# Kernel tuning notes

Measured on AMD Instinct MI355X. Metric: run time of the kernel, lower is better.

## Reference

```python
import jax, jax.numpy as jnp
import numpy as np

D_MODEL = 2048
NUM_HEADS = 32
D_HEAD = D_MODEL // NUM_HEADS
L = 2048


def setup_inputs() -> dict:
    key = jax.random.key(0)
    ks = jax.random.split(key, 9)
    s = 0.02  # init scale
    return {
        "X": jax.random.normal(ks[0], (L, D_MODEL), dtype=jnp.float32),
        "Wq_w": jax.random.normal(ks[1], (D_MODEL, D_MODEL), jnp.float32) * s,
        "Wq_b": jax.random.normal(ks[2], (D_MODEL,), jnp.float32) * s,
        "Wk_w": jax.random.normal(ks[3], (D_MODEL, D_MODEL), jnp.float32) * s,
        "Wk_b": jax.random.normal(ks[4], (D_MODEL,), jnp.float32) * s,
        "Wv_w": jax.random.normal(ks[5], (D_MODEL, D_MODEL), jnp.float32) * s,
        "Wv_b": jax.random.normal(ks[6], (D_MODEL,), jnp.float32) * s,
        "Wo_w": jax.random.normal(ks[7], (D_MODEL, D_MODEL), jnp.float32) * s,
        "Wo_b": jax.random.normal(ks[8], (D_MODEL,), jnp.float32) * s,
    }


def reference(X, Wq_w, Wq_b, Wk_w, Wk_b, Wv_w, Wv_b, Wo_w, Wo_b):
    # torch.nn.Linear: y = x @ W.T + b
    seq = X.shape[0]
    Q = (X @ Wq_w.T + Wq_b).reshape(seq, D_HEAD, NUM_HEADS)  # (L, d, h)
    K = (X @ Wk_w.T + Wk_b).reshape(seq, D_HEAD, NUM_HEADS)
    V = (X @ Wv_w.T + Wv_b).reshape(seq, D_HEAD, NUM_HEADS)
    # scores[l, m, h] = sum_d Q[l,d,h] * K[m,d,h]; note scale is sqrt(d_model),
    # faithful to the source (not sqrt(d_head)).
    scores = jnp.einsum('ldh,mdh->lmh', Q, K) / jnp.sqrt(jnp.float32(D_MODEL))
    attn = jax.nn.softmax(scores, axis=1)  # softmax over key axis m
    out = jnp.einsum('lmh,mdh->ldh', attn, V).reshape(seq, D_MODEL)
    return out @ Wo_w.T + Wo_b
```

## Files before the change

### kernel.cpp

```cpp
#include <hip/hip_runtime.h>
#include <hip/hip_bf16.h>
#include <stdint.h>
#include <stddef.h>

#define L_SEQ   2048
#define DM      2048
#define NH      32
#define DH      64
#define QSCALE  0.02209708691207961f
#define QS2     0.0318793579f
#define MAT_N   (L_SEQ * DM)

typedef __bf16  bf16x8 __attribute__((ext_vector_type(8)));
typedef float   f32x4  __attribute__((ext_vector_type(4)));
typedef __hip_bfloat16 bf16;

#if __has_builtin(__builtin_amdgcn_exp2f)
#define EXP2F(x) __builtin_amdgcn_exp2f(x)
#else
#define EXP2F(x) __expf((x) * 0.6931471805599453f)
#endif

__device__ __forceinline__ void gl_lds16(const bf16* g, bf16* l) {
    __builtin_amdgcn_global_load_lds(
        (const __attribute__((address_space(1))) unsigned int*)g,
        (__attribute__((address_space(3))) unsigned int*)l,
        16, 0, 0);
}

__device__ __forceinline__ void conv8s(const float* src, bf16* dst, int i, float sc) {
    float4 a = *(const float4*)(src + i);
    float4 b = *(const float4*)(src + i + 4);
    union { bf16 h[8]; uint4 u; } pk;
    pk.h[0] = __float2bfloat16(a.x * sc); pk.h[1] = __float2bfloat16(a.y * sc);
    pk.h[2] = __float2bfloat16(a.z * sc); pk.h[3] = __float2bfloat16(a.w * sc);
    pk.h[4] = __float2bfloat16(b.x * sc); pk.h[5] = __float2bfloat16(b.y * sc);
    pk.h[6] = __float2bfloat16(b.z * sc); pk.h[7] = __float2bfloat16(b.w * sc);
    *(uint4*)(dst + i) = pk.u;
}

__global__ __launch_bounds__(256)
void convert4_kernel(const float* __restrict__ s0, const float* __restrict__ s1,
                     const float* __restrict__ s2, const float* __restrict__ s3,
                     bf16* __restrict__ d0, bf16* __restrict__ d1,
                     bf16* __restrict__ d2, bf16* __restrict__ d3)
{
    const float* s; bf16* d; float sc = 1.0f;
    switch (blockIdx.y) {
        case 0:  s = s0; d = d0; break;
        case 1:  s = s1; d = d1; sc = QS2; break;
        case 2:  s = s2; d = d2; break;
        default: s = s3; d = d3; break;
    }
    const int i = (blockIdx.x * 256 + threadIdx.x) * 8;
    conv8s(s, d, i, sc);
}

__global__ __launch_bounds__(256)
void convert_wo_perm_kernel(const float* __restrict__ s, bf16* __restrict__ d)
{
    const int t   = blockIdx.x * 256 + threadIdx.x;
    const int row = t >> 8;
    const int k0  = (t & 255) * 8;
    const float* sr = s + (size_t)row * DM;
    union { bf16 h[8]; uint4 u; } pk;
#pragma unroll
    for (int j = 0; j < 8; ++j) {
        const int kp = k0 + j;
        const int k  = ((kp & 63) << 5) | (kp >> 6);
        pk.h[j] = __float2bfloat16(sr[k]);
    }
    *(uint4*)(d + (size_t)row * DM + k0) = pk.u;
}

__global__ __launch_bounds__(512)
void qkv8_gemm_kernel(const bf16* __restrict__ Xb,
                      const bf16* __restrict__ Wq, const float* __restrict__ bq,
                      const bf16* __restrict__ Wk, const float* __restrict__ bk,
                      const bf16* __restrict__ Wv, const float* __restrict__ bv,
                      bf16* __restrict__ Qws, bf16* __restrict__ Kws, bf16* __restrict__ Vws)
{
    __shared__ bf16 lds[2 * 32768];

    const int bid = blockIdx.x;
    const int mt  = bid & 7;
    const int nt  = bid >> 3;
    const int m0  = mt << 8;
    const int ng0 = nt << 8;
    const int z   = ng0 >> 11;
    const int n0  = ng0 & 2047;
    const bf16*  W    = (z == 0) ? Wq : (z == 1) ? Wk : Wv;
    const float* bias = (z == 0) ? bq : (z == 1) ? bk : bv;

    const int tid  = threadIdx.x;
    const int lane = tid & 63;
    const int wave = tid >> 6;
    const int wm   = wave >> 2;
    const int wn   = wave & 3;
    const int grp8 = (lane >> 4) * 8;
    const int grp4 = (lane >> 4) * 4;
    const int l15  = lane & 15;
    const int axor = (l15 & 7) << 3;

    const int scol = ((tid & 7) * 8) ^ (((tid >> 3) & 7) << 3);
    const bf16* gb[8];
    int loff[8];
#pragma unroll
    for (int e = 0; e < 8; ++e) {
        const int hh  = e >> 1;
        const int row = (e & 1) * 64 + (tid >> 3);
        loff[e] = hh * 8192 + (e & 1) * 4096 + tid * 8;
        if (hh < 2) {
            gb[e] = Xb + (size_t)(m0 + hh * 128 + row) * DM + scol;
        } else {
            const int nn   = n0 + (hh - 2) * 128 + row;
            const int brow = ((nn & 63) << 5) | (nn >> 6);
            gb[e] = W + (size_t)brow * DM + scol;
        }
    }

    const bool swap  = (z == 2);
    const int  aside = swap ? 16384 : 0;
    const int  bside = swap ? 0 : 16384;
    const bf16* fa0 = lds + aside + wm * 8192 + l15 * 64;
    const bf16* fb0 = lds + bside + (wn >> 1) * 8192 + ((wn & 1) * 64 + l15) * 64;

    f32x4 acc[8][4];
    const f32x4 zero = {0.f, 0.f, 0.f, 0.f};
#pragma unroll
    for (int i = 0; i < 8; ++i)
#pragma unroll
        for (int j = 0; j < 4; ++j) acc[i][j] = zero;

#pragma unroll
    for (int e = 0; e < 8; ++e) gl_lds16(gb[e],      lds + loff[e]);
#pragma unroll
    for (int e = 0; e < 8; ++e) gl_lds16(gb[e] + 64, lds + 32768 + loff[e]);
    asm volatile("s_waitcnt vmcnt(8)" ::: "memory");
    asm volatile("s_barrier" ::: "memory");

    for (int t = 0; t < 32; ++t) {
        const int cb = (t & 1) << 15;
        const bf16* fa = fa0 + cb;
        const bf16* fb = fb0 + cb;
        const int c0 = grp8 ^ axor;
        const int c1 = (32 + grp8) ^ axor;

        bf16x8 af[8], bfr[4];
#pragma unroll
        for (int i = 0; i < 8; ++i) af[i] = *(const bf16x8*)(fa + i * 1024 + c0);
#pragma unroll
        for (int j = 0; j < 4; ++j) bfr[j] = *(const bf16x8*)(fb + j * 1024 + c0);
        asm volatile("s_barrier" ::: "memory");
        __builtin_amdgcn_s_setprio(1);
#pragma unroll
        for (int i = 0; i < 8; ++i)
#pragma unroll
            for (int j = 0; j < 4; ++j)
                acc[i][j] = __builtin_amdgcn_mfma_f32_16x16x32_bf16(af[i], bfr[j], acc[i][j], 0, 0, 0);
        __builtin_amdgcn_s_setprio(0);

#pragma unroll
        for (int i = 0; i < 8; ++i) af[i] = *(const bf16x8*)(fa + i * 1024 + c1);
#pragma unroll
        for (int j = 0; j < 4; ++j) bfr[j] = *(const bf16x8*)(fb + j * 1024 + c1);
        asm volatile("s_waitcnt lgkmcnt(0)" ::: "memory");
        asm volatile("s_barrier" ::: "memory");
        if (t + 2 < 32) {
            const int kb2 = (t + 2) << 6;
#pragma unroll
            for (int e = 0; e < 8; ++e)
                gl_lds16(gb[e] + kb2, lds + cb + loff[e]);
            asm volatile("s_waitcnt vmcnt(8)" ::: "memory");
        } else if (t == 30) {
            asm volatile("s_waitcnt vmcnt(0)" ::: "memory");
        }
        __builtin_amdgcn_s_setprio(1);
#pragma unroll
        for (int i = 0; i < 8; ++i)
#pragma unroll
            for (int j = 0; j < 4; ++j)
                acc[i][j] = __builtin_amdgcn_mfma_f32_16x16x32_bf16(af[i], bfr[j], acc[i][j], 0, 0, 0);
        __builtin_amdgcn_s_setprio(0);
        asm volatile("s_barrier" ::: "memory");
    }

    if (z == 0) {
#pragma unroll
        for (int j = 0; j < 4; ++j) {
            const int np = n0 + wn * 64 + j * 16 + l15;
            const float bb = bias[((np & 63) << 5) | (np >> 6)] * QS2;
            const size_t base = ((size_t)(np >> 6) * L_SEQ) * DH + (np & 63);
#pragma unroll
            for (int i = 0; i < 8; ++i)
#pragma unroll
                for (int r = 0; r < 4; ++r) {
                    const int m = m0 + wm * 128 + i * 16 + grp4 + r;
                    Qws[base + (size_t)m * DH] = __float2bfloat16(acc[i][j][r] + bb);
                }
        }
    } else if (z == 1) {
#pragma unroll
        for (int j = 0; j < 4; ++j) {
            const int np = n0 + wn * 64 + j * 16 + l15;
            const float bb = bias[((np & 63) << 5) | (np >> 6)];
            const size_t base = ((size_t)(np >> 6) * L_SEQ) * DH + (np & 63);
#pragma unroll
            for (int i = 0; i < 8; ++i)
#pragma unroll
                for (int r = 0; r < 4; ++r) {
                    const int m = m0 + wm * 128 + i * 16 + grp4 + r;
                    Kws[base + (size_t)m * DH] = __float2bfloat16(acc[i][j][r] + bb);
                }
        }
    } else {
#pragma unroll
        for (int i = 0; i < 8; ++i)
#pragma unroll
            for (int r = 0; r < 4; ++r) {
                const int np = n0 + wm * 128 + i * 16 + grp4 + r;
                const float bb = bias[((np & 63) << 5) | (np >> 6)];
#pragma unroll
                for (int j = 0; j < 4; ++j) {
                    const int mcol = m0 + wn * 64 + j * 16 + l15;
                    Vws[(size_t)np * L_SEQ + mcol] = __float2bfloat16(acc[i][j][r] + bb);
                }
            }
    }
}

__global__ __launch_bounds__(256)
void out8_gemm_kernel(const bf16* __restrict__ A,
                      const bf16* __restrict__ Wo,
                      float* __restrict__ P0, float* __restrict__ P1)
{
    __shared__ bf16 lds[2 * 16384];

    const int m0 = blockIdx.y * 128, n0 = blockIdx.x * 128;
    const int kz = blockIdx.z;
    float* P = kz ? P1 : P0;
    const int kbase = kz * 1024;

    const int tid  = threadIdx.x;
    const int lane = tid & 63;
    const int wave = tid >> 6;
    const int wr   = (wave >> 1) * 64;
    const int wc   = (wave & 1) * 64;
    const int grp8 = (lane >> 4) * 8;
    const int grp4 = (lane >> 4) * 4;
    const int l15  = lane & 15;
    const int axor = (l15 & 7) << 3;

    const bf16* gb[8]; int loff[8];
#pragma unroll
    for (int e = 0; e < 8; ++e) {
        const int idx = (e & 3) * 256 + tid;
        const int row = idx >> 3;
        const int sc  = ((idx & 7) * 8) ^ ((row & 7) << 3);
        if (e < 4) { gb[e] = A  + (size_t)(m0 + row) * DM + kbase + sc; loff[e] = idx * 8; }
        else       { gb[e] = Wo + (size_t)(n0 + row) * DM + kbase + sc; loff[e] = 8192 + idx * 8; }
    }

    f32x4 acc[4][4];
    const f32x4 zero = {0.f, 0.f, 0.f, 0.f};
#pragma unroll
    for (int i = 0; i < 4; ++i)
#pragma unroll
        for (int j = 0; j < 4; ++j) acc[i][j] = zero;

#pragma unroll
    for (int e = 0; e < 8; ++e) gl_lds16(gb[e],      lds + loff[e]);
#pragma unroll
    for (int e = 0; e < 8; ++e) gl_lds16(gb[e] + 64, lds + 16384 + loff[e]);
    asm volatile("s_waitcnt vmcnt(8)" ::: "memory");
    asm volatile("s_barrier" ::: "memory");

    for (int t = 0; t < 16; ++t) {
        const int cb = (t & 1) << 14;
        const bf16* fa = lds + cb;
        const bf16* fb = lds + cb + 8192;
        const int c0 = grp8 ^ axor;
        const int c1 = (32 + grp8) ^ axor;

        bf16x8 af[4], bfr[4];
#pragma unroll
        for (int i = 0; i < 4; ++i) af[i]  = *(const bf16x8*)(fa + (wr + i * 16 + l15) * 64 + c0);
#pragma unroll
        for (int j = 0; j < 4; ++j) bfr[j] = *(const bf16x8*)(fb + (wc + j * 16 + l15) * 64 + c0);
        asm volatile("s_barrier" ::: "memory");
        __builtin_amdgcn_s_setprio(1);
#pragma unroll
        for (int i = 0; i < 4; ++i)
#pragma unroll
            for (int j = 0; j < 4; ++j)
                acc[i][j] = __builtin_amdgcn_mfma_f32_16x16x32_bf16(af[i], bfr[j], acc[i][j], 0, 0, 0);
        __builtin_amdgcn_s_setprio(0);

#pragma unroll
        for (int i = 0; i < 4; ++i) af[i]  = *(const bf16x8*)(fa + (wr + i * 16 + l15) * 64 + c1);
#pragma unroll
        for (int j = 0; j < 4; ++j) bfr[j] = *(const bf16x8*)(fb + (wc + j * 16 + l15) * 64 + c1);
        asm volatile("s_waitcnt lgkmcnt(0)" ::: "memory");
        asm volatile("s_barrier" ::: "memory");
        if (t + 2 < 16) {
            const int kadv = (t + 2) * 64;
#pragma unroll
            for (int e = 0; e < 8; ++e) gl_lds16(gb[e] + kadv, lds + cb + loff[e]);
            asm volatile("s_waitcnt vmcnt(8)" ::: "memory");
        } else if (t == 14) {
            asm volatile("s_waitcnt vmcnt(0)" ::: "memory");
        }
        __builtin_amdgcn_s_setprio(1);
#pragma unroll
        for (int i = 0; i < 4; ++i)
#pragma unroll
            for (int j = 0; j < 4; ++j)
                acc[i][j] = __builtin_amdgcn_mfma_f32_16x16x32_bf16(af[i], bfr[j], acc[i][j], 0, 0, 0);
        __builtin_amdgcn_s_setprio(0);
        asm volatile("s_barrier" ::: "memory");
    }

#pragma unroll
    for (int j = 0; j < 4; ++j) {
        const int n = n0 + wc + j * 16 + l15;
#pragma unroll
        for (int i = 0; i < 4; ++i) {
#pragma unroll
            for (int r = 0; r < 4; ++r) {
                const int m = m0 + wr + i * 16 + grp4 + r;
                P[(size_t)m * DM + n] = acc[i][j][r];
            }
        }
    }
}

__global__ __launch_bounds__(256)
void bias_sum_kernel(const float* __restrict__ P0, const float* __restrict__ P1,
                     const float* __restrict__ bo, float* __restrict__ out)
{
    const int i = (blockIdx.x * 256 + threadIdx.x) * 4;
    float4 a = *(const float4*)(P0 + i);
    float4 b = *(const float4*)(P1 + i);
    float4 c = *(const float4*)(bo + (i & (DM - 1)));
    float4 o;
    o.x = a.x + b.x + c.x; o.y = a.y + b.y + c.y;
    o.z = a.z + b.z + c.z; o.w = a.w + b.w + c.w;
    *(float4*)(out + i) = o;
}

__global__ __launch_bounds__(512)
void attention_kernel(const bf16* __restrict__ Qws,
                      const bf16* __restrict__ Kws,
                      const bf16* __restrict__ Vws,
                      bf16* __restrict__ Attn)
{
    __shared__ bf16 lds[24576];

    const int h = blockIdx.x, qb = blockIdx.y;
    const int tid  = threadIdx.x;
    const int wave = tid >> 6;
    const int lane = tid & 63;
    const int grp  = lane >> 4;
    const int l15  = lane & 15;
    const int grp8 = grp * 8;
    const int axor = (l15 & 7) << 3;

    const bf16* Qh = Qws + (size_t)h * L_SEQ * DH;
    const bf16* Kh = Kws + (size_t)h * L_SEQ * DH;
    const bf16* Vh = Vws + (size_t)h * DH * L_SEQ;

    const int q0 = qb * 128 + wave * 16;

    bf16x8 qf0 = *(const bf16x8*)(Qh + (size_t)(q0 + l15) * DH + grp8);
    bf16x8 qf1 = *(const bf16x8*)(Qh + (size_t)(q0 + l15) * DH + 32 + grp8);

    const int srow = tid >> 3;
    const int scol = ((tid & 7) * 8) ^ ((srow & 7) << 3);
    const bf16* gK = Kh + (size_t)srow * DH + scol;
    const bf16* gV = Vh + (size_t)srow * L_SEQ + scol;
    bf16* ldsK = lds + tid * 8;
    bf16* ldsV = lds + 8192 + tid * 8;
    bf16* Plds = lds + 16384;
    const int prow = (wave * 16 + l15) * 64;

    const f32x4 zero = {0.f, 0.f, 0.f, 0.f};
    f32x4 Oacc[4];
#pragma unroll
    for (int t = 0; t < 4; ++t) Oacc[t] = zero;
    float lsum = 0.f;

    gl_lds16(gK,        ldsK);
    gl_lds16(gV,        ldsV);
    gl_lds16(gK + 4096, ldsK + 4096);
    gl_lds16(gV + 64,   ldsV + 4096);
    asm volatile("s_waitcnt vmcnt(2)" ::: "memory");
    asm volatile("s_barrier" ::: "memory");

    for (int kb = 0; kb < 32; ++kb) {
        const int cb = (kb & 1) << 12;
        const bf16* Kc = lds + cb;
        const bf16* Vc = lds + 8192 + cb;

#pragma unroll
        for (int t = 0; t < 4; ++t) {
            const int rr = (t * 16 + l15) * 64;
            bf16x8 k0 = *(const bf16x8*)(Kc + rr + (grp8 ^ axor));
            bf16x8 k1 = *(const bf16x8*)(Kc + rr + ((32 + grp8) ^ axor));
            f32x4 s = zero;
            __builtin_amdgcn_s_setprio(1);
            s = __builtin_amdgcn_mfma_f32_16x16x32_bf16(k0, qf0, s, 0, 0, 0);
            s = __builtin_amdgcn_mfma_f32_16x16x32_bf16(k1, qf1, s, 0, 0, 0);
            __builtin_amdgcn_s_setprio(0);
            float p0 = EXP2F(s[0]), p1 = EXP2F(s[1]),
                  p2 = EXP2F(s[2]), p3 = EXP2F(s[3]);
            lsum += (p0 + p1) + (p2 + p3);
            union { bf16 hh[4]; uint2 u; } pk;
            pk.hh[0] = __float2bfloat16(p0); pk.hh[1] = __float2bfloat16(p1);
            pk.hh[2] = __float2bfloat16(p2); pk.hh[3] = __float2bfloat16(p3);
            *(uint2*)(&Plds[prow + ((t * 16 + grp * 4) ^ axor)]) = pk.u;
        }
        asm volatile("s_waitcnt lgkmcnt(0)" ::: "memory");

        __builtin_amdgcn_s_setprio(1);
#pragma unroll
        for (int ks = 0; ks < 2; ++ks) {
            bf16x8 pa = *(const bf16x8*)(&Plds[prow + ((ks * 32 + grp8) ^ axor)]);
#pragma unroll
            for (int t = 0; t < 4; ++t) {
                bf16x8 vb = *(const bf16x8*)(Vc + (t * 16 + l15) * 64 + ((ks * 32 + grp8) ^ axor));
                Oacc[t] = __builtin_amdgcn_mfma_f32_16x16x32_bf16(pa, vb, Oacc[t], 0, 0, 0);
            }
        }
        __builtin_amdgcn_s_setprio(0);

        asm volatile("s_waitcnt lgkmcnt(0)" ::: "memory");
        asm volatile("s_barrier" ::: "memory");
        if (kb + 2 < 32) {
            gl_lds16(gK + (kb + 2) * 4096, ldsK + cb);
            gl_lds16(gV + (kb + 2) * 64,   ldsV + cb);
            asm volatile("s_waitcnt vmcnt(2)" ::: "memory");
        } else if (kb == 30) {
            asm volatile("s_waitcnt vmcnt(0)" ::: "memory");
        }
        asm volatile("s_barrier" ::: "memory");
    }

    float sden = lsum;
    sden += __shfl_xor(sden, 16, 64);
    sden += __shfl_xor(sden, 32, 64);
    const float inv = 1.f / sden;
    float invs[4];
#pragma unroll
    for (int r = 0; r < 4; ++r)
        invs[r] = __shfl(inv, grp * 4 + r, 64);

#pragma unroll
    for (int t = 0; t < 4; ++t) {
#pragma unroll
        for (int r = 0; r < 4; ++r) {
            const int m = q0 + grp * 4 + r;
            const int d = t * 16 + l15;
            Attn[(size_t)m * DM + h * 64 + d] = __float2bfloat16(Oacc[t][r] * invs[r]);
        }
    }
}

extern "C" void kernel_launch(void* const* d_in, const int* in_sizes, int n_in,
                              void* d_out, int out_size, void* d_ws, size_t ws_size,
                              hipStream_t stream)
{
    const float* X  = (const float*)d_in[0];
    const float* Wq = (const float*)d_in[1];
    const float* bq = (const float*)d_in[2];
    const float* Wk = (const float*)d_in[3];
    const float* bk = (const float*)d_in[4];
    const float* Wv = (const float*)d_in[5];
    const float* bv = (const float*)d_in[6];
    const float* Wo = (const float*)d_in[7];
    const float* bo = (const float*)d_in[8];
    float* out = (float*)d_out;

    bf16* Xb   = (bf16*)d_ws;
    bf16* Wqb  = Xb  + (size_t)MAT_N;
    bf16* Wkb  = Wqb + (size_t)MAT_N;
    bf16* Wvb  = Wkb + (size_t)MAT_N;
    bf16* Qws  = Wvb + (size_t)MAT_N;
    bf16* Kws  = Qws + (size_t)MAT_N;
    bf16* Vws  = Kws + (size_t)MAT_N;
    bf16* Wob  = Xb;
    bf16* Attn = Wqb;
    float* P0  = (float*)Wkb;
    float* P1  = (float*)Qws;

    convert4_kernel<<<dim3(2048, 4), 256, 0, stream>>>(X, Wq, Wk, Wv, Xb, Wqb, Wkb, Wvb);
    qkv8_gemm_kernel<<<dim3(192), 512, 0, stream>>>(Xb, Wqb, bq, Wkb, bk, Wvb, bv,
                                                    Qws, Kws, Vws);
    convert_wo_perm_kernel<<<dim3(2048), 256, 0, stream>>>(Wo, Wob);
    attention_kernel<<<dim3(32, 16), 512, 0, stream>>>(Qws, Kws, Vws, Attn);
    out8_gemm_kernel<<<dim3(16, 16, 2), 256, 0, stream>>>(Attn, Wob, P0, P1);
    bias_sum_kernel<<<dim3(4096), 256, 0, stream>>>(P0, P1, bo, out);
}
```

Before: 263.8 us.

## Split QKV GEMM fragment loads into quarters and double attention rows per wave

In the QKV GEMM, each K-half is now processed in two smaller A-fragment groups that reuse one B fragment set. This lowers register pressure but adds extra barriers and LDS waits. The attention kernel now runs with 256 threads, and each wave handles 32 query rows instead of 16, so each K/V fragment read from LDS feeds two MFMAs. Each thread issues twice the global-to-LDS loads, and fewer waves per block may reduce latency hiding.

```diff
diff --git a/kernel.cpp b/kernel.cpp
--- a/kernel.cpp
+++ b/kernel.cpp
@@ -146,24 +146,53 @@
         const int c0 = grp8 ^ axor;
         const int c1 = (32 + grp8) ^ axor;
 
-        bf16x8 af[8], bfr[4];
-#pragma unroll
-        for (int i = 0; i < 8; ++i) af[i] = *(const bf16x8*)(fa + i * 1024 + c0);
-#pragma unroll
-        for (int j = 0; j < 4; ++j) bfr[j] = *(const bf16x8*)(fb + j * 1024 + c0);
-        asm volatile("s_barrier" ::: "memory");
-        __builtin_amdgcn_s_setprio(1);
-#pragma unroll
-        for (int i = 0; i < 8; ++i)
+        bf16x8 a0[4], a1[4], b0[4];
+
+#pragma unroll
+        for (int i = 0; i < 4; ++i) a0[i] = *(const bf16x8*)(fa + i * 1024 + c0);
+#pragma unroll
+        for (int j = 0; j < 4; ++j) b0[j] = *(const bf16x8*)(fb + j * 1024 + c0);
+        asm volatile("s_barrier" ::: "memory");
+        asm volatile("s_waitcnt lgkmcnt(0)" ::: "memory");
+        __builtin_amdgcn_s_setprio(1);
+#pragma unroll
+        for (int i = 0; i < 4; ++i)
 #pragma unroll
             for (int j = 0; j < 4; ++j)
-                acc[i][j] = __builtin_amdgcn_mfma_f32_16x16x32_bf16(af[i], bfr[j], acc[i][j], 0, 0, 0);
-        __builtin_amdgcn_s_setprio(0);
-
-#pragma unroll
-        for (int i = 0; i < 8; ++i) af[i] = *(const bf16x8*)(fa + i * 1024 + c1);
-#pragma unroll
-        for (int j = 0; j < 4; ++j) bfr[j] = *(const bf16x8*)(fb + j * 1024 + c1);
+                acc[i][j] = __builtin_amdgcn_mfma_f32_16x16x32_bf16(a0[i], b0[j], acc[i][j], 0, 0, 0);
+        __builtin_amdgcn_s_setprio(0);
+        asm volatile("s_barrier" ::: "memory");
+
+#pragma unroll
+        for (int i = 0; i < 4; ++i) a1[i] = *(const bf16x8*)(fa + (4 + i) * 1024 + c0);
+        asm volatile("s_barrier" ::: "memory");
+        asm volatile("s_waitcnt lgkmcnt(0)" ::: "memory");
+        __builtin_amdgcn_s_setprio(1);
+#pragma unroll
+        for (int i = 0; i < 4; ++i)
+#pragma unroll
+            for (int j = 0; j < 4; ++j)
+                acc[4 + i][j] = __builtin_amdgcn_mfma_f32_16x16x32_bf16(a1[i], b0[j], acc[4 + i][j], 0, 0, 0);
+        __builtin_amdgcn_s_setprio(0);
+        asm volatile("s_barrier" ::: "memory");
+
+#pragma unroll
+        for (int i = 0; i < 4; ++i) a0[i] = *(const bf16x8*)(fa + i * 1024 + c1);
+#pragma unroll
+        for (int j = 0; j < 4; ++j) b0[j] = *(const bf16x8*)(fb + j * 1024 + c1);
+        asm volatile("s_barrier" ::: "memory");
+        asm volatile("s_waitcnt lgkmcnt(0)" ::: "memory");
+        __builtin_amdgcn_s_setprio(1);
+#pragma unroll
+        for (int i = 0; i < 4; ++i)
+#pragma unroll
+            for (int j = 0; j < 4; ++j)
+                acc[i][j] = __builtin_amdgcn_mfma_f32_16x16x32_bf16(a0[i], b0[j], acc[i][j], 0, 0, 0);
+        __builtin_amdgcn_s_setprio(0);
+        asm volatile("s_barrier" ::: "memory");
+
+#pragma unroll
+        for (int i = 0; i < 4; ++i) a1[i] = *(const bf16x8*)(fa + (4 + i) * 1024 + c1);
         asm volatile("s_waitcnt lgkmcnt(0)" ::: "memory");
         asm volatile("s_barrier" ::: "memory");
         if (t + 2 < 32) {
@@ -177,10 +206,10 @@
         }
         __builtin_amdgcn_s_setprio(1);
 #pragma unroll
-        for (int i = 0; i < 8; ++i)
+        for (int i = 0; i < 4; ++i)
 #pragma unroll
             for (int j = 0; j < 4; ++j)
-                acc[i][j] = __builtin_amdgcn_mfma_f32_16x16x32_bf16(af[i], bfr[j], acc[i][j], 0, 0, 0);
+                acc[4 + i][j] = __builtin_amdgcn_mfma_f32_16x16x32_bf16(a1[i], b0[j], acc[4 + i][j], 0, 0, 0);
         __builtin_amdgcn_s_setprio(0);
         asm volatile("s_barrier" ::: "memory");
     }
@@ -348,7 +377,7 @@
     *(float4*)(out + i) = o;
 }
 
-__global__ __launch_bounds__(512)
+__global__ __launch_bounds__(256)
 void attention_kernel(const bf16* __restrict__ Qws,
                       const bf16* __restrict__ Kws,
                       const bf16* __restrict__ Vws,
@@ -369,31 +398,47 @@
     const bf16* Kh = Kws + (size_t)h * L_SEQ * DH;
     const bf16* Vh = Vws + (size_t)h * DH * L_SEQ;
 
-    const int q0 = qb * 128 + wave * 16;
-
-    bf16x8 qf0 = *(const bf16x8*)(Qh + (size_t)(q0 + l15) * DH + grp8);
-    bf16x8 qf1 = *(const bf16x8*)(Qh + (size_t)(q0 + l15) * DH + 32 + grp8);
-
-    const int srow = tid >> 3;
-    const int scol = ((tid & 7) * 8) ^ ((srow & 7) << 3);
-    const bf16* gK = Kh + (size_t)srow * DH + scol;
-    const bf16* gV = Vh + (size_t)srow * L_SEQ + scol;
-    bf16* ldsK = lds + tid * 8;
-    bf16* ldsV = lds + 8192 + tid * 8;
+    const int q0 = qb * 128 + wave * 32;
+
+    bf16x8 qf[2][2];
+#pragma unroll
+    for (int g = 0; g < 2; ++g) {
+        qf[g][0] = *(const bf16x8*)(Qh + (size_t)(q0 + g * 16 + l15) * DH + grp8);
+        qf[g][1] = *(const bf16x8*)(Qh + (size_t)(q0 + g * 16 + l15) * DH + 32 + grp8);
+    }
+
+    const bf16* gK[2]; const bf16* gV[2]; int soff[2];
+#pragma unroll
+    for (int r = 0; r < 2; ++r) {
+        const int c   = r * 256 + tid;
+        const int row = c >> 3;
+        const int sc  = ((c & 7) * 8) ^ ((row & 7) << 3);
+        gK[r] = Kh + (size_t)row * DH + sc;
+        gV[r] = Vh + (size_t)row * L_SEQ + sc;
+        soff[r] = c * 8;
+    }
+    bf16* ldsK = lds;
+    bf16* ldsV = lds + 8192;
     bf16* Plds = lds + 16384;
-    const int prow = (wave * 16 + l15) * 64;
+    int prow[2];
+    prow[0] = (wave * 32 + l15) * 64;
+    prow[1] = (wave * 32 + 16 + l15) * 64;
 
     const f32x4 zero = {0.f, 0.f, 0.f, 0.f};
-    f32x4 Oacc[4];
-#pragma unroll
-    for (int t = 0; t < 4; ++t) Oacc[t] = zero;
-    float lsum = 0.f;
-
-    gl_lds16(gK,        ldsK);
-    gl_lds16(gV,        ldsV);
-    gl_lds16(gK + 4096, ldsK + 4096);
-    gl_lds16(gV + 64,   ldsV + 4096);
-    asm volatile("s_waitcnt vmcnt(2)" ::: "memory");
+    f32x4 Oacc[2][4];
+#pragma unroll
+    for (int g = 0; g < 2; ++g)
+#pragma unroll
+        for (int t = 0; t < 4; ++t) Oacc[g][t] = zero;
+    float lsum[2] = {0.f, 0.f};
+
+#pragma unroll
+    for (int r = 0; r < 2; ++r) { gl_lds16(gK[r],        ldsK + soff[r]);
+                                  gl_lds16(gV[r],        ldsV + soff[r]); }
+#pragma unroll
+    for (int r = 0; r < 2; ++r) { gl_lds16(gK[r] + 4096, ldsK + 4096 + soff[r]);
+                                  gl_lds16(gV[r] + 64,   ldsV + 4096 + soff[r]); }
+    asm volatile("s_waitcnt vmcnt(4)" ::: "memory");
     asm volatile("s_barrier" ::: "memory");
 
     for (int kb = 0; kb < 32; ++kb) {
@@ -406,29 +451,34 @@
             const int rr = (t * 16 + l15) * 64;
             bf16x8 k0 = *(const bf16x8*)(Kc + rr + (grp8 ^ axor));
             bf16x8 k1 = *(const bf16x8*)(Kc + rr + ((32 + grp8) ^ axor));
-            f32x4 s = zero;
-            __builtin_amdgcn_s_setprio(1);
-            s = __builtin_amdgcn_mfma_f32_16x16x32_bf16(k0, qf0, s, 0, 0, 0);
-            s = __builtin_amdgcn_mfma_f32_16x16x32_bf16(k1, qf1, s, 0, 0, 0);
-            __builtin_amdgcn_s_setprio(0);
-            float p0 = EXP2F(s[0]), p1 = EXP2F(s[1]),
-                  p2 = EXP2F(s[2]), p3 = EXP2F(s[3]);
-            lsum += (p0 + p1) + (p2 + p3);
-            union { bf16 hh[4]; uint2 u; } pk;
-            pk.hh[0] = __float2bfloat16(p0); pk.hh[1] = __float2bfloat16(p1);
-            pk.hh[2] = __float2bfloat16(p2); pk.hh[3] = __float2bfloat16(p3);
-            *(uint2*)(&Plds[prow + ((t * 16 + grp * 4) ^ axor)]) = pk.u;
+#pragma unroll
+            for (int g = 0; g < 2; ++g) {
+                f32x4 s = zero;
+                __builtin_amdgcn_s_setprio(1);
+                s = __builtin_amdgcn_mfma_f32_16x16x32_bf16(k0, qf[g][0], s, 0, 0, 0);
+                s = __builtin_amdgcn_mfma_f32_16x16x32_bf16(k1, qf[g][1], s, 0, 0, 0);
+                __builtin_amdgcn_s_setprio(0);
+                float p0 = EXP2F(s[0]), p1 = EXP2F(s[1]),
+                      p2 = EXP2F(s[2]), p3 = EXP2F(s[3]);
+                lsum[g] += (p0 + p1) + (p2 + p3);
+                union { bf16 hh[4]; uint2 u; } pk;
+                pk.hh[0] = __float2bfloat16(p0); pk.hh[1] = __float2bfloat16(p1);
+                pk.hh[2] = __float2bfloat16(p2); pk.hh[3] = __float2bfloat16(p3);
+                *(uint2*)(&Plds[prow[g] + ((t * 16 + grp * 4) ^ axor)]) = pk.u;
+            }
         }
         asm volatile("s_waitcnt lgkmcnt(0)" ::: "memory");
 
         __builtin_amdgcn_s_setprio(1);
 #pragma unroll
         for (int ks = 0; ks < 2; ++ks) {
-            bf16x8 pa = *(const bf16x8*)(&Plds[prow + ((ks * 32 + grp8) ^ axor)]);
+            bf16x8 pa0 = *(const bf16x8*)(&Plds[prow[0] + ((ks * 32 + grp8) ^ axor)]);
+            bf16x8 pa1 = *(const bf16x8*)(&Plds[prow[1] + ((ks * 32 + grp8) ^ axor)]);
 #pragma unroll
             for (int t = 0; t < 4; ++t) {
                 bf16x8 vb = *(const bf16x8*)(Vc + (t * 16 + l15) * 64 + ((ks * 32 + grp8) ^ axor));
-                Oacc[t] = __builtin_amdgcn_mfma_f32_16x16x32_bf16(pa, vb, Oacc[t], 0, 0, 0);
+                Oacc[0][t] = __builtin_amdgcn_mfma_f32_16x16x32_bf16(pa0, vb, Oacc[0][t], 0, 0, 0);
+                Oacc[1][t] = __builtin_amdgcn_mfma_f32_16x16x32_bf16(pa1, vb, Oacc[1][t], 0, 0, 0);
             }
         }
         __builtin_amdgcn_s_setprio(0);
@@ -436,31 +486,37 @@
         asm volatile("s_waitcnt lgkmcnt(0)" ::: "memory");
         asm volatile("s_barrier" ::: "memory");
         if (kb + 2 < 32) {
-            gl_lds16(gK + (kb + 2) * 4096, ldsK + cb);
-            gl_lds16(gV + (kb + 2) * 64,   ldsV + cb);
-            asm volatile("s_waitcnt vmcnt(2)" ::: "memory");
+#pragma unroll
+            for (int r = 0; r < 2; ++r) {
+                gl_lds16(gK[r] + (kb + 2) * 4096, ldsK + cb + soff[r]);
+                gl_lds16(gV[r] + (kb + 2) * 64,   ldsV + cb + soff[r]);
+            }
+            asm volatile("s_waitcnt vmcnt(4)" ::: "memory");
         } else if (kb == 30) {
             asm volatile("s_waitcnt vmcnt(0)" ::: "memory");
         }
         asm volatile("s_barrier" ::: "memory");
     }
 
-    float sden = lsum;
-    sden += __shfl_xor(sden, 16, 64);
-    sden += __shfl_xor(sden, 32, 64);
-    const float inv = 1.f / sden;
-    float invs[4];
-#pragma unroll
-    for (int r = 0; r < 4; ++r)
-        invs[r] = __shfl(inv, grp * 4 + r, 64);
-
-#pragma unroll
-    for (int t = 0; t < 4; ++t) {
-#pragma unroll
-        for (int r = 0; r < 4; ++r) {
-            const int m = q0 + grp * 4 + r;
-            const int d = t * 16 + l15;
-            Attn[(size_t)m * DM + h * 64 + d] = __float2bfloat16(Oacc[t][r] * invs[r]);
+#pragma unroll
+    for (int g = 0; g < 2; ++g) {
+        float sden = lsum[g];
+        sden += __shfl_xor(sden, 16, 64);
+        sden += __shfl_xor(sden, 32, 64);
+        const float inv = 1.f / sden;
+        float invs[4];
+#pragma unroll
+        for (int r = 0; r < 4; ++r)
+            invs[r] = __shfl(inv, grp * 4 + r, 64);
+
+#pragma unroll
+        for (int t = 0; t < 4; ++t) {
+#pragma unroll
+            for (int r = 0; r < 4; ++r) {
+                const int m = q0 + g * 16 + grp * 4 + r;
+                const int d = t * 16 + l15;
+                Attn[(size_t)m * DM + h * 64 + d] = __float2bfloat16(Oacc[g][t][r] * invs[r]);
+            }
         }
     }
 }
@@ -496,7 +552,7 @@
     qkv8_gemm_kernel<<<dim3(192), 512, 0, stream>>>(Xb, Wqb, bq, Wkb, bk, Wvb, bv,
                                                     Qws, Kws, Vws);
     convert_wo_perm_kernel<<<dim3(2048), 256, 0, stream>>>(Wo, Wob);
-    attention_kernel<<<dim3(32, 16), 512, 0, stream>>>(Qws, Kws, Vws, Attn);
+    attention_kernel<<<dim3(32, 16), 256, 0, stream>>>(Qws, Kws, Vws, Attn);
     out8_gemm_kernel<<<dim3(16, 16, 2), 256, 0, stream>>>(Attn, Wob, P0, P1);
     bias_sum_kernel<<<dim3(4096), 256, 0, stream>>>(P0, P1, bo, out);
 }
```

Result: slower. 274.8 us (+4.2%).

## Fuse Wo conversion into QKV GEMM and bias into single-pass output GEMM

Applied to the files above, without the earlier changes.

When the workspace is large enough, the Wo fp32-to-bf16 permuted conversion runs in 64 extra blocks appended to the QKV GEMM launch, filling otherwise idle CUs on a 256-CU part, and writes to a separate buffer. The output projection drops its split-K into two fp32 partials plus a separate bias-sum kernel. It now does the full K loop in one 512-thread kernel with 128x128 tiles and adds the bias in the epilogue. This removes two launches and the partial-buffer round trip, at the cost of half as many output blocks (256) and a longer serial K loop per block.

```diff
diff --git a/kernel.cpp b/kernel.cpp
--- a/kernel.cpp
+++ b/kernel.cpp
@@ -78,11 +78,34 @@
                       const bf16* __restrict__ Wq, const float* __restrict__ bq,
                       const bf16* __restrict__ Wk, const float* __restrict__ bk,
                       const bf16* __restrict__ Wv, const float* __restrict__ bv,
-                      bf16* __restrict__ Qws, bf16* __restrict__ Kws, bf16* __restrict__ Vws)
+                      bf16* __restrict__ Qws, bf16* __restrict__ Kws, bf16* __restrict__ Vws,
+                      const float* __restrict__ WoSrc, bf16* __restrict__ WobDst)
 {
     __shared__ bf16 lds[2 * 32768];
 
     const int bid = blockIdx.x;
+    const int tid  = threadIdx.x;
+
+    if (bid >= 192) {
+        const int t = (bid - 192) * 512 + tid;
+        const int row = t >> 4;
+        const int k0base = (t & 15) * 128;
+        const float* sr = WoSrc + (size_t)row * DM;
+        bf16* dr = WobDst + (size_t)row * DM;
+        for (int i = 0; i < 16; ++i) {
+            const int k0 = k0base + i * 8;
+            union { bf16 h[8]; uint4 u; } pk;
+#pragma unroll
+            for (int j = 0; j < 8; ++j) {
+                const int kp = k0 + j;
+                const int k  = ((kp & 63) << 5) | (kp >> 6);
+                pk.h[j] = __float2bfloat16(sr[k]);
+            }
+            *(uint4*)(dr + k0) = pk.u;
+        }
+        return;
+    }
+
     const int mt  = bid & 7;
     const int nt  = bid >> 3;
     const int m0  = mt << 8;
@@ -92,7 +115,6 @@
     const bf16*  W    = (z == 0) ? Wq : (z == 1) ? Wk : Wv;
     const float* bias = (z == 0) ? bq : (z == 1) ? bk : bv;
 
-    const int tid  = threadIdx.x;
     const int lane = tid & 63;
     const int wave = tid >> 6;
     const int wm   = wave >> 2;
@@ -229,90 +251,87 @@
     }
 }
 
-__global__ __launch_bounds__(256)
-void out8_gemm_kernel(const bf16* __restrict__ A,
+__global__ __launch_bounds__(512)
+void out_fused_kernel(const bf16* __restrict__ A,
                       const bf16* __restrict__ Wo,
-                      float* __restrict__ P0, float* __restrict__ P1)
+                      const float* __restrict__ bo,
+                      float* __restrict__ out)
 {
     __shared__ bf16 lds[2 * 16384];
 
     const int m0 = blockIdx.y * 128, n0 = blockIdx.x * 128;
-    const int kz = blockIdx.z;
-    float* P = kz ? P1 : P0;
-    const int kbase = kz * 1024;
-
     const int tid  = threadIdx.x;
     const int lane = tid & 63;
     const int wave = tid >> 6;
-    const int wr   = (wave >> 1) * 64;
-    const int wc   = (wave & 1) * 64;
+    const int wm   = wave >> 1;
+    const int wn   = wave & 1;
     const int grp8 = (lane >> 4) * 8;
     const int grp4 = (lane >> 4) * 4;
     const int l15  = lane & 15;
     const int axor = (l15 & 7) << 3;
 
-    const bf16* gb[8]; int loff[8];
-#pragma unroll
-    for (int e = 0; e < 8; ++e) {
-        const int idx = (e & 3) * 256 + tid;
+    const bf16* gb[4]; int loff[4];
+#pragma unroll
+    for (int e = 0; e < 4; ++e) {
+        const int idx = (e & 1) * 512 + tid;
         const int row = idx >> 3;
         const int sc  = ((idx & 7) * 8) ^ ((row & 7) << 3);
-        if (e < 4) { gb[e] = A  + (size_t)(m0 + row) * DM + kbase + sc; loff[e] = idx * 8; }
-        else       { gb[e] = Wo + (size_t)(n0 + row) * DM + kbase + sc; loff[e] = 8192 + idx * 8; }
-    }
-
-    f32x4 acc[4][4];
+        if (e < 2) { gb[e] = A  + (size_t)(m0 + row) * DM + sc; loff[e] = idx * 8; }
+        else       { gb[e] = Wo + (size_t)(n0 + row) * DM + sc; loff[e] = 8192 + idx * 8; }
+    }
+
+    f32x4 acc[2][4];
     const f32x4 zero = {0.f, 0.f, 0.f, 0.f};
 #pragma unroll
-    for (int i = 0; i < 4; ++i)
+    for (int i = 0; i < 2; ++i)
 #pragma unroll
         for (int j = 0; j < 4; ++j) acc[i][j] = zero;
 
 #pragma unroll
-    for (int e = 0; e < 8; ++e) gl_lds16(gb[e],      lds + loff[e]);
-#pragma unroll
-    for (int e = 0; e < 8; ++e) gl_lds16(gb[e] + 64, lds + 16384 + loff[e]);
-    asm volatile("s_waitcnt vmcnt(8)" ::: "memory");
+    for (int e = 0; e < 4; ++e) gl_lds16(gb[e],      lds + loff[e]);
+#pragma unroll
+    for (int e = 0; e < 4; ++e) gl_lds16(gb[e] + 64, lds + 16384 + loff[e]);
+    asm volatile("s_waitcnt vmcnt(4)" ::: "memory");
     asm volatile("s_barrier" ::: "memory");
 
-    for (int t = 0; t < 16; ++t) {
+    for (int t = 0; t < 32; ++t) {
         const int cb = (t & 1) << 14;
         const bf16* fa = lds + cb;
         const bf16* fb = lds + cb + 8192;
         const int c0 = grp8 ^ axor;
         const int c1 = (32 + grp8) ^ axor;
 
-        bf16x8 af[4], bfr[4];
-#pragma unroll
-        for (int i = 0; i < 4; ++i) af[i]  = *(const bf16x8*)(fa + (wr + i * 16 + l15) * 64 + c0);
-#pragma unroll
-        for (int j = 0; j < 4; ++j) bfr[j] = *(const bf16x8*)(fb + (wc + j * 16 + l15) * 64 + c0);
+        bf16x8 af[2], bfr[4];
+#pragma unroll
+        for (int i = 0; i < 2; ++i) af[i]  = *(const bf16x8*)(fa + (wm * 32 + i * 16 + l15) * 64 + c0);
+#pragma unroll
+        for (int j = 0; j < 4; ++j) bfr[j] = *(const bf16x8*)(fb + (wn * 64 + j * 16 + l15) * 64 + c0);
         asm volatile("s_barrier" ::: "memory");
         __builtin_amdgcn_s_setprio(1);
 #pragma unroll
-        for (int i = 0; i < 4; ++i)
+        for (int i = 0; i < 2; ++i)
 #pragma unroll
             for (int j = 0; j < 4; ++j)
                 acc[i][j] = __builtin_amdgcn_mfma_f32_16x16x32_bf16(af[i], bfr[j], acc[i][j], 0, 0, 0);
         __builtin_amdgcn_s_setprio(0);
 
 #pragma unroll
-        for (int i = 0; i < 4; ++i) af[i]  = *(const bf16x8*)(fa + (wr + i * 16 + l15) * 64 + c1);
-#pragma unroll
-        for (int j = 0; j < 4; ++j) bfr[j] = *(const bf16x8*)(fb + (wc + j * 16 + l15) * 64 + c1);
+        for (int i = 0; i < 2; ++i) af[i]  = *(const bf16x8*)(fa + (wm * 32 + i * 16 + l15) * 64 + c1);
+#pragma unroll
+        for (int j = 0; j < 4; ++j) bfr[j] = *(const bf16x8*)(fb + (wn * 64 + j * 16 + l15) * 64 + c1);
         asm volatile("s_waitcnt lgkmcnt(0)" ::: "memory");
         asm volatile("s_barrier" ::: "memory");
-        if (t + 2 < 16) {
+        if (t + 2 < 32) {
             const int kadv = (t + 2) * 64;
 #pragma unroll
-            for (int e = 0; e < 8; ++e) gl_lds16(gb[e] + kadv, lds + cb + loff[e]);
-            asm volatile("s_waitcnt vmcnt(8)" ::: "memory");
-        } else if (t == 14) {
+            for (int e = 0; e < 4; ++e) gl_lds16(gb[e] + kadv, lds + cb + loff[e]);
+            asm volatile("s_waitcnt vmcnt(4)" ::: "memory");
+        } else if (t == 30) {
             asm volatile("s_waitcnt vmcnt(0)" ::: "memory");
         }
         __builtin_amdgcn_s_setprio(1);
 #pragma unroll
-        for (int i = 0; i < 4; ++i)
+        for (int i = 0; i < 2; ++i)
 #pragma unroll
             for (int j = 0; j < 4; ++j)
                 acc[i][j] = __builtin_amdgcn_mfma_f32_16x16x32_bf16(af[i], bfr[j], acc[i][j], 0, 0, 0);
@@ -322,30 +341,17 @@
 
 #pragma unroll
     for (int j = 0; j < 4; ++j) {
-        const int n = n0 + wc + j * 16 + l15;
-#pragma unroll
-        for (int i = 0; i < 4; ++i) {
+        const int n = n0 + wn * 64 + j * 16 + l15;
+        const float bb = bo[n];
+#pragma unroll
+        for (int i = 0; i < 2; ++i) {
 #pragma unroll
             for (int r = 0; r < 4; ++r) {
-                const int m = m0 + wr + i * 16 + grp4 + r;
-                P[(size_t)m * DM + n] = acc[i][j][r];
+                const int m = m0 + wm * 32 + i * 16 + grp4 + r;
+                out[(size_t)m * DM + n] = acc[i][j][r] + bb;
             }
         }
     }
-}
-
-__global__ __launch_bounds__(256)
-void bias_sum_kernel(const float* __restrict__ P0, const float* __restrict__ P1,
-                     const float* __restrict__ bo, float* __restrict__ out)
-{
-    const int i = (blockIdx.x * 256 + threadIdx.x) * 4;
-    float4 a = *(const float4*)(P0 + i);
-    float4 b = *(const float4*)(P1 + i);
-    float4 c = *(const float4*)(bo + (i & (DM - 1)));
-    float4 o;
-    o.x = a.x + b.x + c.x; o.y = a.y + b.y + c.y;
-    o.z = a.z + b.z + c.z; o.w = a.w + b.w + c.w;
-    *(float4*)(out + i) = o;
 }
 
 __global__ __launch_bounds__(512)
@@ -487,16 +493,21 @@
     bf16* Qws  = Wvb + (size_t)MAT_N;
     bf16* Kws  = Qws + (size_t)MAT_N;
     bf16* Vws  = Kws + (size_t)MAT_N;
-    bf16* Wob  = Xb;
+    bf16* Wob7 = Vws + (size_t)MAT_N;
     bf16* Attn = Wqb;
-    float* P0  = (float*)Wkb;
-    float* P1  = (float*)Qws;
+
+    const bool big = ws_size >= (size_t)8 * MAT_N * sizeof(bf16);
+    bf16* Wob = big ? Wob7 : Xb;
 
     convert4_kernel<<<dim3(2048, 4), 256, 0, stream>>>(X, Wq, Wk, Wv, Xb, Wqb, Wkb, Wvb);
-    qkv8_gemm_kernel<<<dim3(192), 512, 0, stream>>>(Xb, Wqb, bq, Wkb, bk, Wvb, bv,
-                                                    Qws, Kws, Vws);
-    convert_wo_perm_kernel<<<dim3(2048), 256, 0, stream>>>(Wo, Wob);
+    if (big) {
+        qkv8_gemm_kernel<<<dim3(256), 512, 0, stream>>>(Xb, Wqb, bq, Wkb, bk, Wvb, bv,
+                                                        Qws, Kws, Vws, Wo, Wob7);
+    } else {
+        qkv8_gemm_kernel<<<dim3(192), 512, 0, stream>>>(Xb, Wqb, bq, Wkb, bk, Wvb, bv,
+                                                        Qws, Kws, Vws, Wo, Wob);
+        convert_wo_perm_kernel<<<dim3(2048), 256, 0, stream>>>(Wo, Wob);
+    }
     attention_kernel<<<dim3(32, 16), 512, 0, stream>>>(Qws, Kws, Vws, Attn);
-    out8_gemm_kernel<<<dim3(16, 16, 2), 256, 0, stream>>>(Attn, Wob, P0, P1);
-    bias_sum_kernel<<<dim3(4096), 256, 0, stream>>>(P0, P1, bo, out);
-}
+    out_fused_kernel<<<dim3(16, 16), 512, 0, stream>>>(Attn, Wob, bo, out);
+}
```

Result: faster. 249.7 us (-5.3%).
